# Optimization experiments

Measured on AMD Instinct MI355X. Metric: run time of the kernel, lower is better.

## Reference

```python
import jax, jax.numpy as jnp
import numpy as np

VOCAB = 32000
EMB = 1024


def setup_inputs() -> dict:
    key = jax.random.key(0)
    k1, k2 = jax.random.split(key)
    tokens = jax.random.randint(k1, (8, 4096), 0, VOCAB, dtype=jnp.int64 if jax.config.jax_enable_x64 else jnp.int32)
    # nn.Linear(vocab, emb, bias=False) weight: [emb, vocab]
    W = jax.random.normal(k2, (EMB, VOCAB), dtype=jnp.float32) * (1.0 / np.sqrt(VOCAB))
    return {"tokens": tokens, "W": W}


def reference(tokens, W):
    # Original: one_hot(tokens, vocab) @ W.T  ==  gather columns of W
    # out[b, s, :] = W[:, tokens[b, s]]
    return W.T[tokens]  # [B, S, EMB]
```

## Files before the change

### kernel.cpp

```cpp
#include <hip/hip_runtime.h>

#define VOCAB 32000
#define EMB   1024
#define TPB   512
#define COLS  32
#define TILES (VOCAB / COLS)
#define CH    512
#define NCHUNK (EMB / CH)
#define CAP_T 256

typedef float f32x4 __attribute__((ext_vector_type(4)));

__global__ __launch_bounds__(TPB) void tok_emb_zero(int* __restrict__ cnt) {
    const int i = blockIdx.x * TPB + threadIdx.x;
    if (i < TILES) cnt[i] = 0;
}

__global__ __launch_bounds__(TPB) void tok_emb_bucket(
    const int* __restrict__ tokens, int* __restrict__ cnt,
    int* __restrict__ bucket, int n_tokens) {
    const int i4 = (blockIdx.x * TPB + threadIdx.x) * 4;
    if (i4 + 3 < n_tokens) {
        const int4 tk = *reinterpret_cast<const int4*>(&tokens[i4]);
        const int tv[4] = {tk.x, tk.y, tk.z, tk.w};
#pragma unroll
        for (int j = 0; j < 4; ++j) {
            const unsigned tile = (unsigned)tv[j] >> 5;
            if (tile < TILES) {
                const int p = atomicAdd(&cnt[tile], 1);
                if (p < CAP_T) bucket[tile * CAP_T + p] = ((i4 + j) << 5) | (tv[j] & 31);
            }
        }
    } else {
        for (int i = i4; i < n_tokens; ++i) {
            const unsigned tile = (unsigned)tokens[i] >> 5;
            if (tile < TILES) {
                const int p = atomicAdd(&cnt[tile], 1);
                if (p < CAP_T) bucket[tile * CAP_T + p] = (i << 5) | (tokens[i] & 31);
            }
        }
    }
}

__global__ __launch_bounds__(TPB) void tok_emb_main(
    const float* __restrict__ W, const int* __restrict__ tokens,
    const int* __restrict__ cnt, const int* __restrict__ bucket,
    f32x4* __restrict__ out4, int n_tokens) {
    __shared__ float lds[COLS * CH];
    __shared__ int   list[CAP_T];
    __shared__ int   scnt;

    const int tile = blockIdx.x;
    const int v0   = tile * COLS;
    const int tid  = threadIdx.x;

    const int cg  = tid & 7;
    const int rb  = tid >> 3;
    const int swz = cg << 2;

    const float* wbase = W + (size_t)v0 + (size_t)(cg << 2);

    f32x4 r[8];
    auto issue = [&](int c0) {
#pragma unroll
        for (int k = 0; k < 8; ++k)
            r[k] = *reinterpret_cast<const f32x4*>(
                wbase + (size_t)(c0 + rb + (k << 6)) * VOCAB);
    };
    auto commit = [&]() {
#pragma unroll
        for (int k = 0; k < 8; ++k) {
            const int rs = (rb + (k << 6)) ^ swz;
#pragma unroll
            for (int j = 0; j < 4; ++j)
                lds[(((cg << 2) + j) << 9) + rs] = r[k][j];
        }
    };

    auto process = [&](int m) {
        if (m == 0) return;
        issue(0);
        commit();
        __syncthreads();
        for (int ch = 0; ch < NCHUNK; ++ch) {
            if (ch + 1 < NCHUNK) issue((ch + 1) * CH);
            const int c0  = ch * CH;
            const int nst = m << 7;
            for (int j = tid; j < nst; j += TPB) {
                const int ent = list[j >> 7];
                const int i   = j & 127;
                const int t   = ent >> 5;
                const int c   = ent & 31;
                const f32x4 v = *reinterpret_cast<const f32x4*>(
                    lds + (c << 9) + ((i << 2) ^ ((c >> 2) << 2)));
                __builtin_nontemporal_store(
                    v, &out4[(size_t)t * (EMB / 4) + (c0 >> 2) + i]);
            }
            __syncthreads();
            if (ch + 1 < NCHUNK) {
                commit();
                __syncthreads();
            }
        }
    };

    const int m_total = (bucket != nullptr) ? cnt[tile] : CAP_T + 1;
    if (m_total <= CAP_T) {
        for (int j = tid; j < m_total; j += TPB)
            list[j] = bucket[tile * CAP_T + j];
        process(m_total);
    } else {
        for (int lo = 0; lo < n_tokens; lo += CAP_T) {
            const int hi = (lo + CAP_T < n_tokens) ? lo + CAP_T : n_tokens;
            __syncthreads();
            if (tid == 0) scnt = 0;
            __syncthreads();
            for (int i = lo + tid; i < hi; i += TPB) {
                const unsigned d = (unsigned)(tokens[i] - v0);
                if (d < COLS) {
                    const int p = atomicAdd(&scnt, 1);
                    list[p] = (i << 5) | (int)d;
                }
            }
            __syncthreads();
            process(scnt);
        }
    }
}

extern "C" void kernel_launch(void* const* d_in, const int* in_sizes, int n_in,
                              void* d_out, int out_size, void* d_ws, size_t ws_size,
                              hipStream_t stream) {
    const int*   tokens   = (const int*)d_in[0];
    const float* W        = (const float*)d_in[1];
    f32x4*       out4     = (f32x4*)d_out;
    const int    n_tokens = in_sizes[0];

    const size_t need = (size_t)TILES * sizeof(int)
                      + (size_t)TILES * CAP_T * sizeof(int);
    if (ws_size >= need) {
        int* cnt    = (int*)d_ws;
        int* bucket = cnt + TILES;
        tok_emb_zero<<<(TILES + TPB - 1) / TPB, TPB, 0, stream>>>(cnt);
        const int quads = (n_tokens + 3) / 4;
        tok_emb_bucket<<<(quads + TPB - 1) / TPB, TPB, 0, stream>>>(
            tokens, cnt, bucket, n_tokens);
        tok_emb_main<<<TILES, TPB, 0, stream>>>(
            W, tokens, cnt, bucket, out4, n_tokens);
    } else {
        tok_emb_main<<<TILES, TPB, 0, stream>>>(
            W, tokens, nullptr, nullptr, out4, n_tokens);
    }
}
```

Measured before the change: 60.55 us.

## Widen vocab tiles to 256 columns and split embedding rows across blocks

Measured after the change: 86.70 us. +43.2%, slower.

```diff
diff --git a/kernel.cpp b/kernel.cpp
--- a/kernel.cpp
+++ b/kernel.cpp
@@ -2,41 +2,41 @@
 
 #define VOCAB 32000
 #define EMB   1024
-#define TPB   512
-#define COLS  32
+#define TPB   1024
+#define COLS  256
 #define TILES (VOCAB / COLS)
-#define CH    512
-#define NCHUNK (EMB / CH)
-#define CAP_T 256
+#define RG    256
+#define NRG   (EMB / RG)
+#define CH    128
+#define CAP_T 512
 
 typedef float f32x4 __attribute__((ext_vector_type(4)));
 
-__global__ __launch_bounds__(TPB) void tok_emb_zero(int* __restrict__ cnt) {
-    const int i = blockIdx.x * TPB + threadIdx.x;
-    if (i < TILES) cnt[i] = 0;
+__global__ __launch_bounds__(256) void tok_emb_zero(int* __restrict__ cnt) {
+    if (threadIdx.x < TILES) cnt[threadIdx.x] = 0;
 }
 
-__global__ __launch_bounds__(TPB) void tok_emb_bucket(
+__global__ __launch_bounds__(256) void tok_emb_bucket(
     const int* __restrict__ tokens, int* __restrict__ cnt,
     int* __restrict__ bucket, int n_tokens) {
-    const int i4 = (blockIdx.x * TPB + threadIdx.x) * 4;
+    const int i4 = (blockIdx.x * 256 + threadIdx.x) * 4;
     if (i4 + 3 < n_tokens) {
         const int4 tk = *reinterpret_cast<const int4*>(&tokens[i4]);
         const int tv[4] = {tk.x, tk.y, tk.z, tk.w};
 #pragma unroll
         for (int j = 0; j < 4; ++j) {
-            const unsigned tile = (unsigned)tv[j] >> 5;
+            const unsigned tile = (unsigned)tv[j] >> 8;
             if (tile < TILES) {
                 const int p = atomicAdd(&cnt[tile], 1);
-                if (p < CAP_T) bucket[tile * CAP_T + p] = ((i4 + j) << 5) | (tv[j] & 31);
+                if (p < CAP_T) bucket[tile * CAP_T + p] = ((i4 + j) << 8) | (tv[j] & 255);
             }
         }
     } else {
         for (int i = i4; i < n_tokens; ++i) {
-            const unsigned tile = (unsigned)tokens[i] >> 5;
+            const unsigned tile = (unsigned)tokens[i] >> 8;
             if (tile < TILES) {
                 const int p = atomicAdd(&cnt[tile], 1);
-                if (p < CAP_T) bucket[tile * CAP_T + p] = (i << 5) | (tokens[i] & 31);
+                if (p < CAP_T) bucket[tile * CAP_T + p] = (i << 8) | (tokens[i] & 255);
             }
         }
     }
@@ -50,65 +50,63 @@
     __shared__ int   list[CAP_T];
     __shared__ int   scnt;
 
-    const int tile = blockIdx.x;
-    const int v0   = tile * COLS;
-    const int tid  = threadIdx.x;
+    const int tile  = blockIdx.x % TILES;
+    const int rg    = blockIdx.x / TILES;
+    const int v0    = tile * COLS;
+    const int rbase = rg * RG;
+    const int tid   = threadIdx.x;
 
-    const int cg  = tid & 7;
-    const int rb  = tid >> 3;
-    const int swz = cg << 2;
+    const int g   = tid & 63;
+    const int r0  = tid >> 6;
+    const int swz = (g & 7) << 2;
 
-    const float* wbase = W + (size_t)v0 + (size_t)(cg << 2);
+    const float* wbase = W + (size_t)v0 + (size_t)(g << 2);
 
-    f32x4 r[8];
+    f32x4 rv[8];
     auto issue = [&](int c0) {
 #pragma unroll
         for (int k = 0; k < 8; ++k)
-            r[k] = *reinterpret_cast<const f32x4*>(
-                wbase + (size_t)(c0 + rb + (k << 6)) * VOCAB);
+            rv[k] = *reinterpret_cast<const f32x4*>(
+                wbase + (size_t)(rbase + c0 + r0 + (k << 4)) * VOCAB);
     };
     auto commit = [&]() {
 #pragma unroll
         for (int k = 0; k < 8; ++k) {
-            const int rs = (rb + (k << 6)) ^ swz;
+            const int rs = (r0 + (k << 4)) ^ swz;
 #pragma unroll
             for (int j = 0; j < 4; ++j)
-                lds[(((cg << 2) + j) << 9) + rs] = r[k][j];
+                lds[((g << 2) + j) * CH + rs] = rv[k][j];
         }
     };
-
-    auto process = [&](int m) {
-        if (m == 0) return;
-        issue(0);
-        commit();
-        __syncthreads();
-        for (int ch = 0; ch < NCHUNK; ++ch) {
-            if (ch + 1 < NCHUNK) issue((ch + 1) * CH);
-            const int c0  = ch * CH;
-            const int nst = m << 7;
-            for (int j = tid; j < nst; j += TPB) {
-                const int ent = list[j >> 7];
-                const int i   = j & 127;
-                const int t   = ent >> 5;
-                const int c   = ent & 31;
-                const f32x4 v = *reinterpret_cast<const f32x4*>(
-                    lds + (c << 9) + ((i << 2) ^ ((c >> 2) << 2)));
-                __builtin_nontemporal_store(
-                    v, &out4[(size_t)t * (EMB / 4) + (c0 >> 2) + i]);
-            }
-            __syncthreads();
-            if (ch + 1 < NCHUNK) {
-                commit();
-                __syncthreads();
-            }
+    auto wphase = [&](int m, int ch) {
+        const int base4 = (rbase + ch * CH) >> 2;
+        const int nst = m << 5;
+        for (int j = tid; j < nst; j += TPB) {
+            const int ent = list[j >> 5];
+            const int i   = j & 31;
+            const int t   = ent >> 8;
+            const int c   = ent & 255;
+            const f32x4 v = *reinterpret_cast<const f32x4*>(
+                lds + c * CH + ((i << 2) ^ (((c >> 2) & 7) << 2)));
+            __builtin_nontemporal_store(
+                v, &out4[(size_t)t * (EMB / 4) + base4 + i]);
         }
     };
 
     const int m_total = (bucket != nullptr) ? cnt[tile] : CAP_T + 1;
     if (m_total <= CAP_T) {
+        issue(0);
         for (int j = tid; j < m_total; j += TPB)
             list[j] = bucket[tile * CAP_T + j];
-        process(m_total);
+        commit();
+        __syncthreads();
+        if (m_total == 0) return;
+        issue(CH);
+        wphase(m_total, 0);
+        __syncthreads();
+        commit();
+        __syncthreads();
+        wphase(m_total, 1);
     } else {
         for (int lo = 0; lo < n_tokens; lo += CAP_T) {
             const int hi = (lo + CAP_T < n_tokens) ? lo + CAP_T : n_tokens;
@@ -119,11 +117,22 @@
                 const unsigned d = (unsigned)(tokens[i] - v0);
                 if (d < COLS) {
                     const int p = atomicAdd(&scnt, 1);
-                    list[p] = (i << 5) | (int)d;
+                    list[p] = (i << 8) | (int)d;
                 }
             }
             __syncthreads();
-            process(scnt);
+            const int m = scnt;
+            if (m) {
+                issue(0);
+                commit();
+                __syncthreads();
+                issue(CH);
+                wphase(m, 0);
+                __syncthreads();
+                commit();
+                __syncthreads();
+                wphase(m, 1);
+            }
         }
     }
 }
@@ -141,14 +150,14 @@
     if (ws_size >= need) {
         int* cnt    = (int*)d_ws;
         int* bucket = cnt + TILES;
-        tok_emb_zero<<<(TILES + TPB - 1) / TPB, TPB, 0, stream>>>(cnt);
+        tok_emb_zero<<<1, 256, 0, stream>>>(cnt);
         const int quads = (n_tokens + 3) / 4;
-        tok_emb_bucket<<<(quads + TPB - 1) / TPB, TPB, 0, stream>>>(
+        tok_emb_bucket<<<(quads + 255) / 256, 256, 0, stream>>>(
             tokens, cnt, bucket, n_tokens);
-        tok_emb_main<<<TILES, TPB, 0, stream>>>(
+        tok_emb_main<<<TILES * NRG, TPB, 0, stream>>>(
             W, tokens, cnt, bucket, out4, n_tokens);
     } else {
-        tok_emb_main<<<TILES, TPB, 0, stream>>>(
+        tok_emb_main<<<TILES * NRG, TPB, 0, stream>>>(
             W, tokens, nullptr, nullptr, out4, n_tokens);
     }
 }
```

## Fuse token bucketing into main kernel via per-block token scan

Applied to the files above, without the earlier changes.

Result: faster. 55.75 us, median of 2 (-7.9%).

```diff
diff --git a/kernel.cpp b/kernel.cpp
--- a/kernel.cpp
+++ b/kernel.cpp
@@ -7,47 +7,15 @@
 #define TILES (VOCAB / COLS)
 #define CH    512
 #define NCHUNK (EMB / CH)
-#define CAP_T 256
+#define CAP   256
 
 typedef float f32x4 __attribute__((ext_vector_type(4)));
 
-__global__ __launch_bounds__(TPB) void tok_emb_zero(int* __restrict__ cnt) {
-    const int i = blockIdx.x * TPB + threadIdx.x;
-    if (i < TILES) cnt[i] = 0;
-}
-
-__global__ __launch_bounds__(TPB) void tok_emb_bucket(
-    const int* __restrict__ tokens, int* __restrict__ cnt,
-    int* __restrict__ bucket, int n_tokens) {
-    const int i4 = (blockIdx.x * TPB + threadIdx.x) * 4;
-    if (i4 + 3 < n_tokens) {
-        const int4 tk = *reinterpret_cast<const int4*>(&tokens[i4]);
-        const int tv[4] = {tk.x, tk.y, tk.z, tk.w};
-#pragma unroll
-        for (int j = 0; j < 4; ++j) {
-            const unsigned tile = (unsigned)tv[j] >> 5;
-            if (tile < TILES) {
-                const int p = atomicAdd(&cnt[tile], 1);
-                if (p < CAP_T) bucket[tile * CAP_T + p] = ((i4 + j) << 5) | (tv[j] & 31);
-            }
-        }
-    } else {
-        for (int i = i4; i < n_tokens; ++i) {
-            const unsigned tile = (unsigned)tokens[i] >> 5;
-            if (tile < TILES) {
-                const int p = atomicAdd(&cnt[tile], 1);
-                if (p < CAP_T) bucket[tile * CAP_T + p] = (i << 5) | (tokens[i] & 31);
-            }
-        }
-    }
-}
-
-__global__ __launch_bounds__(TPB) void tok_emb_main(
+__global__ __launch_bounds__(TPB) void tok_emb_fused(
     const float* __restrict__ W, const int* __restrict__ tokens,
-    const int* __restrict__ cnt, const int* __restrict__ bucket,
     f32x4* __restrict__ out4, int n_tokens) {
     __shared__ float lds[COLS * CH];
-    __shared__ int   list[CAP_T];
+    __shared__ int   list[CAP];
     __shared__ int   scnt;
 
     const int tile = blockIdx.x;
@@ -76,54 +44,79 @@
                 lds[(((cg << 2) + j) << 9) + rs] = r[k][j];
         }
     };
-
-    auto process = [&](int m) {
-        if (m == 0) return;
-        issue(0);
-        commit();
-        __syncthreads();
-        for (int ch = 0; ch < NCHUNK; ++ch) {
-            if (ch + 1 < NCHUNK) issue((ch + 1) * CH);
-            const int c0  = ch * CH;
-            const int nst = m << 7;
-            for (int j = tid; j < nst; j += TPB) {
-                const int ent = list[j >> 7];
-                const int i   = j & 127;
-                const int t   = ent >> 5;
-                const int c   = ent & 31;
-                const f32x4 v = *reinterpret_cast<const f32x4*>(
-                    lds + (c << 9) + ((i << 2) ^ ((c >> 2) << 2)));
-                __builtin_nontemporal_store(
-                    v, &out4[(size_t)t * (EMB / 4) + (c0 >> 2) + i]);
+    auto wphase = [&](int m, int ch) {
+        const int base4 = ch * (CH / 4);
+        const int nst = m << 7;
+        for (int j = tid; j < nst; j += TPB) {
+            const int ent = list[j >> 7];
+            const int i   = j & 127;
+            const int t   = ent >> 5;
+            const int c   = ent & 31;
+            const f32x4 v = *reinterpret_cast<const f32x4*>(
+                lds + (c << 9) + ((i << 2) ^ ((c >> 2) << 2)));
+            __builtin_nontemporal_store(
+                v, &out4[(size_t)t * (EMB / 4) + base4 + i]);
+        }
+    };
+    auto scan = [&](int lo, int hi) {
+        const int nv = (hi - lo) >> 2;
+        for (int q = tid; q < nv; q += TPB) {
+            const int4 tk = *reinterpret_cast<const int4*>(&tokens[lo + (q << 2)]);
+            const int tv[4] = {tk.x, tk.y, tk.z, tk.w};
+#pragma unroll
+            for (int j = 0; j < 4; ++j) {
+                const unsigned d = (unsigned)(tv[j] - v0);
+                if (d < COLS) {
+                    const int p = atomicAdd(&scnt, 1);
+                    if (p < CAP) list[p] = ((lo + (q << 2) + j) << 5) | (int)d;
+                }
             }
-            __syncthreads();
-            if (ch + 1 < NCHUNK) {
-                commit();
-                __syncthreads();
+        }
+        for (int i = lo + (nv << 2) + tid; i < hi; i += TPB) {
+            const unsigned d = (unsigned)(tokens[i] - v0);
+            if (d < COLS) {
+                const int p = atomicAdd(&scnt, 1);
+                if (p < CAP) list[p] = (i << 5) | (int)d;
             }
         }
     };
 
-    const int m_total = (bucket != nullptr) ? cnt[tile] : CAP_T + 1;
-    if (m_total <= CAP_T) {
-        for (int j = tid; j < m_total; j += TPB)
-            list[j] = bucket[tile * CAP_T + j];
-        process(m_total);
+    if (tid == 0) scnt = 0;
+    issue(0);
+    __syncthreads();
+    scan(0, n_tokens);
+    commit();
+    __syncthreads();
+    const int m_total = scnt;
+
+    if (m_total <= CAP) {
+        if (m_total == 0) return;
+        issue(CH);
+        wphase(m_total, 0);
+        __syncthreads();
+        commit();
+        __syncthreads();
+        wphase(m_total, 1);
     } else {
-        for (int lo = 0; lo < n_tokens; lo += CAP_T) {
-            const int hi = (lo + CAP_T < n_tokens) ? lo + CAP_T : n_tokens;
+        for (int lo = 0; lo < n_tokens; lo += CAP) {
+            const int hi = (lo + CAP < n_tokens) ? lo + CAP : n_tokens;
             __syncthreads();
             if (tid == 0) scnt = 0;
             __syncthreads();
-            for (int i = lo + tid; i < hi; i += TPB) {
-                const unsigned d = (unsigned)(tokens[i] - v0);
-                if (d < COLS) {
-                    const int p = atomicAdd(&scnt, 1);
-                    list[p] = (i << 5) | (int)d;
-                }
+            scan(lo, hi);
+            __syncthreads();
+            const int m = scnt;
+            if (m) {
+                issue(0);
+                commit();
+                __syncthreads();
+                issue(CH);
+                wphase(m, 0);
+                __syncthreads();
+                commit();
+                __syncthreads();
+                wphase(m, 1);
             }
-            __syncthreads();
-            process(scnt);
         }
     }
 }
@@ -136,19 +129,5 @@
     f32x4*       out4     = (f32x4*)d_out;
     const int    n_tokens = in_sizes[0];
 
-    const size_t need = (size_t)TILES * sizeof(int)
-                      + (size_t)TILES * CAP_T * sizeof(int);
-    if (ws_size >= need) {
-        int* cnt    = (int*)d_ws;
-        int* bucket = cnt + TILES;
-        tok_emb_zero<<<(TILES + TPB - 1) / TPB, TPB, 0, stream>>>(cnt);
-        const int quads = (n_tokens + 3) / 4;
-        tok_emb_bucket<<<(quads + TPB - 1) / TPB, TPB, 0, stream>>>(
-            tokens, cnt, bucket, n_tokens);
-        tok_emb_main<<<TILES, TPB, 0, stream>>>(
-            W, tokens, cnt, bucket, out4, n_tokens);
-    } else {
-        tok_emb_main<<<TILES, TPB, 0, stream>>>(
-            W, tokens, nullptr, nullptr, out4, n_tokens);
-    }
+    tok_emb_fused<<<TILES, TPB, 0, stream>>>(W, tokens, out4, n_tokens);
 }
```
